# Optimization experiments

Measured on AMD Instinct MI355X. Metric: run time of the kernel, lower is better.

Reference implementation:

```python
import jax, jax.numpy as jnp
import numpy as np

TOPK = 0.1  # fraction of h*w spatial positions, from __init__ default


def setup_inputs() -> dict:
    key = jax.random.key(0)
    x = jax.random.normal(key, (32, 256, 56, 56), dtype=jnp.float32)
    return {"x": x}


def reference(x) -> jnp.ndarray:
    # Faithful translation of TopKLayer.sparse_hw (including its quirky
    # comparison of ascending *ranks* against the spatial *index* of the
    # k-th largest element, exactly as the torch code does).
    n, c, h, w = x.shape
    k = int(max(1, TOPK * h * w))  # topk_keep_num = 313 for 56x56
    x_r = x.reshape(n * c, h * w)              # (nc, hw)
    abs_x = jnp.abs(x_r)
    # ranks[i, j] = ascending rank of abs_x[i, j] within row i
    ranks = jnp.argsort(jnp.argsort(abs_x, axis=1), axis=1)
    # spatial index of the k-th largest |x| in each row
    thr_idx = jax.lax.top_k(abs_x, k)[1][:, -1]  # (nc,)
    mask = (ranks < thr_idx[:, None]).reshape(n, c, h, w)
    return x * mask.astype(x.dtype)
```

## Files before the change

### kernel.cpp

```cpp
#include <hip/hip_runtime.h>
#include <stdint.h>


#define HW     3136
#define NT     128
#define WPB    2
#define KSEL   313u
#define CAP    448
#define CAP2   64
#define SLICE  1088
#define O_CAND 0
#define O_HC   448
#define O_TINY 704
#define M31    0x7fffffffu

__device__ __forceinline__ unsigned wscan_incl(unsigned v) {
    const int lane = threadIdx.x & 63;
#pragma unroll
    for (int d = 1; d < 64; d <<= 1) {
        unsigned o = __shfl_up(v, d, 64);
        if (lane >= d) v += o;
    }
    return v;
}

__device__ __forceinline__ unsigned bcast_first(unsigned flag, unsigned val) {
    unsigned long long bal = __ballot(flag != 0);
    int fl = __ffsll(bal) - 1;
    return __shfl(val, fl, 64);
}

__device__ __forceinline__ void hadd(unsigned* h, unsigned b) {
    atomicAdd(&h[(b >> 1) + (b >> 5)], (b & 1) ? 0x10000u : 1u);
}

template <bool fromTop>
__device__ __forceinline__ void wave_select(
        unsigned* sl, const unsigned* __restrict__ gx,
        const uint4* v, unsigned vx,
        const unsigned* pc, unsigned base,
        unsigned rank, unsigned& keyOut, unsigned& idxOut) {
    const int lane = threadIdx.x & 63;

    unsigned packed1 = 0;
    {
        unsigned run = base;
#pragma unroll
        for (int i = 0; i < 32; ++i) {
            const unsigned cb = (i & 1) ? (pc[i >> 1] >> 16) : (pc[i >> 1] & 0xFFFFu);
            if (fromTop) {
                const unsigned suf = HW - run - cb;
                if (suf < rank && rank <= suf + cb)
                    packed1 = ((unsigned)(lane * 32 + i) << 16) | (rank - suf);
            } else {
                if (run < rank && rank <= run + cb)
                    packed1 = ((unsigned)(lane * 32 + i) << 16) | (rank - run);
            }
            run += cb;
        }
    }
    packed1 = bcast_first(packed1, packed1);
    const unsigned b0 = packed1 >> 16;
    const unsigned m1 = packed1 & 0xFFFFu;

    unsigned cc = 0;
#pragma unroll
    for (int i = 0; i < 12; ++i) {
        cc += (((v[i].x & M31) >> 20) == b0);
        cc += (((v[i].y & M31) >> 20) == b0);
        cc += (((v[i].z & M31) >> 20) == b0);
        cc += (((v[i].w & M31) >> 20) == b0);
    }
    cc += (((vx & M31) >> 20) == b0);
    const unsigned cin = wscan_incl(cc);
    const unsigned cnt = __shfl(cin, 63, 64);
    bool fb = (cnt > CAP);
    unsigned result = 0;

    if (!fb) {
        unsigned pos = cin - cc;
#pragma unroll
        for (int i = 0; i < 12; ++i) {
            const unsigned i0 = 4u * (unsigned)(lane + 64 * i);
            unsigned k;
            k = v[i].x & M31; if ((k >> 20) == b0) sl[O_CAND + pos++] = ((k & 0xFFFFFu) << 12) | i0;
            k = v[i].y & M31; if ((k >> 20) == b0) sl[O_CAND + pos++] = ((k & 0xFFFFFu) << 12) | (i0 + 1u);
            k = v[i].z & M31; if ((k >> 20) == b0) sl[O_CAND + pos++] = ((k & 0xFFFFFu) << 12) | (i0 + 2u);
            k = v[i].w & M31; if ((k >> 20) == b0) sl[O_CAND + pos++] = ((k & 0xFFFFFu) << 12) | (i0 + 3u);
        }
        { const unsigned k = vx & M31;
          if ((k >> 20) == b0) sl[O_CAND + pos++] = ((k & 0xFFFFFu) << 12) | (3072u + (unsigned)lane); }

#pragma unroll
        for (int i = 0; i < 4; ++i) sl[O_HC + lane + 64 * i] = 0;
        for (unsigned i = lane; i < cnt; i += 64)
            atomicAdd(&sl[O_HC + (sl[O_CAND + i] >> 24)], 1u);

        unsigned hh[4];
#pragma unroll
        for (int i = 0; i < 4; ++i) hh[i] = sl[O_HC + 4 * lane + i];
        const unsigned s4 = hh[0] + hh[1] + hh[2] + hh[3];
        unsigned run2 = wscan_incl(s4) - s4;
        unsigned packed2 = 0;
#pragma unroll
        for (int i = 0; i < 4; ++i) {
            if (fromTop) {
                const unsigned suf = cnt - run2 - hh[i];
                if (suf < m1 && m1 <= suf + hh[i])
                    packed2 = ((unsigned)(4 * lane + i) << 16) | (m1 - suf);
            } else {
                if (run2 < m1 && m1 <= run2 + hh[i])
                    packed2 = ((unsigned)(4 * lane + i) << 16) | (m1 - run2);
            }
            run2 += hh[i];
        }
        packed2 = bcast_first(packed2, packed2);
        const unsigned b2 = packed2 >> 16;
        const unsigned m2 = packed2 & 0xFFFFu;

        unsigned tc = 0;
        for (unsigned i = lane; i < cnt; i += 64) tc += ((sl[O_CAND + i] >> 24) == b2);
        const unsigned tincl = wscan_incl(tc);
        const unsigned c2 = __shfl(tincl, 63, 64);
        if (c2 > CAP2) fb = true;
        else {
            unsigned tpos = tincl - tc;
            for (unsigned i = lane; i < cnt; i += 64) {
                const unsigned cw = sl[O_CAND + i];
                if ((cw >> 24) == b2) sl[O_TINY + tpos++] = cw;
            }
            unsigned hitf = 0, resv = 0;
            if ((unsigned)lane < c2) {
                const unsigned ci = sl[O_TINY + lane];
                const unsigned di = fromTop ? (ci ^ 0xFFFu) : ci;
                unsigned r = 1;
                for (unsigned j = 0; j < c2; ++j) {
                    const unsigned dj = fromTop ? (sl[O_TINY + j] ^ 0xFFFu) : sl[O_TINY + j];
                    if (fromTop ? (dj > di) : (dj < di)) r++;
                }
                if (r == m2) { hitf = 1; resv = ci; }
            }
            result = bcast_first(hitf, resv);
        }
    }

    if (fb) {
        unsigned hitf = 0, resv = 0;
        for (unsigned j = lane; j < HW; j += 64) {
            const unsigned k = gx[j] & M31;
            if ((k >> 20) != b0) continue;
            unsigned Ci = ((k & 0xFFFFFu) << 12) | j;
            if (fromTop) Ci ^= 0xFFFu;
            unsigned r = 1;
            for (unsigned j2 = 0; j2 < HW; ++j2) {
                const unsigned k2 = gx[j2] & M31;
                if ((k2 >> 20) != b0) continue;
                unsigned Cj = ((k2 & 0xFFFFFu) << 12) | j2;
                if (fromTop) Cj ^= 0xFFFu;
                if (fromTop ? (Cj > Ci) : (Cj < Ci)) r++;
            }
            if (r == m1) { hitf = 1; resv = ((k & 0xFFFFFu) << 12) | j; }
        }
        result = bcast_first(hitf, resv);
    }

    keyOut = (b0 << 20) | (result >> 12);
    idxOut = result & 0xFFFu;
}

extern "C" __global__ void __launch_bounds__(NT)
topk_kernel(const float* __restrict__ x, float* __restrict__ out) {
    __shared__ unsigned lds[WPB][SLICE];
    const int lane = threadIdx.x & 63;
    const int w = threadIdx.x >> 6;
    const int row = blockIdx.x * WPB + w;
    unsigned* sl = lds[w];
    const uint4* __restrict__ xin4 = (const uint4*)(x + (size_t)row * HW);
    const unsigned* __restrict__ gx = (const unsigned*)xin4;
    uint4* __restrict__ xout4 = (uint4*)(out + (size_t)row * HW);
    unsigned* __restrict__ gout = (unsigned*)(out + (size_t)row * HW);

#pragma unroll
    for (int i = 0; i < 17; ++i) sl[lane + 64 * i] = 0;

    uint4 v[12];
#pragma unroll
    for (int i = 0; i < 12; ++i) v[i] = xin4[lane + 64 * i];
    const unsigned vx = gx[3072 + lane];

#pragma unroll
    for (int i = 0; i < 12; ++i) {
        hadd(sl, (v[i].x & M31) >> 20);
        hadd(sl, (v[i].y & M31) >> 20);
        hadd(sl, (v[i].z & M31) >> 20);
        hadd(sl, (v[i].w & M31) >> 20);
    }
    hadd(sl, (vx & M31) >> 20);

    unsigned pc[16];
#pragma unroll
    for (int i = 0; i < 16; ++i) pc[i] = sl[lane * 17 + i];
    unsigned ssum = 0;
#pragma unroll
    for (int i = 0; i < 16; ++i) ssum += (pc[i] & 0xFFFFu) + (pc[i] >> 16);
    const unsigned base = wscan_incl(ssum) - ssum;

    unsigned KA, tIdx;
    wave_select<true>(sl, gx, v, vx, pc, base, KSEL, KA, tIdx);

    if (tIdx == 0) {
        const uint4 z = make_uint4(0u, 0u, 0u, 0u);
#pragma unroll
        for (int i = 0; i < 12; ++i) xout4[lane + 64 * i] = z;
        gout[3072 + lane] = 0u;
        return;
    }

    unsigned KB, eB;
    wave_select<false>(sl, gx, v, vx, pc, base, tIdx, KB, eB);

#pragma unroll
    for (int i = 0; i < 12; ++i) {
        const unsigned i0 = 4u * (unsigned)(lane + 64 * i);
        uint4 o = v[i];
        unsigned k;
        k = o.x & M31; if (!(k < KB || (k == KB && i0      <= eB))) o.x = 0u;
        k = o.y & M31; if (!(k < KB || (k == KB && i0 + 1u <= eB))) o.y = 0u;
        k = o.z & M31; if (!(k < KB || (k == KB && i0 + 2u <= eB))) o.z = 0u;
        k = o.w & M31; if (!(k < KB || (k == KB && i0 + 3u <= eB))) o.w = 0u;
        xout4[lane + 64 * i] = o;
    }
    {
        const unsigned k = vx & M31;
        gout[3072 + lane] =
            (k < KB || (k == KB && (3072u + (unsigned)lane) <= eB)) ? vx : 0u;
    }
}

extern "C" void kernel_launch(void* const* d_in, const int* in_sizes, int n_in,
                              void* d_out, int out_size, void* d_ws, size_t ws_size,
                              hipStream_t stream) {
    const float* x = (const float*)d_in[0];
    float* out = (float*)d_out;
    const int rows = in_sizes[0] / HW;
    topk_kernel<<<dim3(rows / WPB), dim3(NT), 0, stream>>>(x, out);
}
```

Before: 63.48 us.

## Process two rows per 256-thread block with block-wide radix histograms

Replaces the one-wavefront-per-row design with a 256-thread block that handles two rows jointly. Each row gets a 2048-bin histogram on the top 11 key bits, built with block-wide LDS atomics, and the two rows' bin counts are packed into 16-bit halves so a single prefix scan covers both. Candidate compaction now uses atomic counters, the refinement step runs on one wave per row, and the fallback is spread across the whole block. The goal is to cut per-thread register load and serial per-wave work, at the cost of extra __syncthreads barriers and atomic contention.

```diff
diff --git a/kernel.cpp b/kernel.cpp
--- a/kernel.cpp
+++ b/kernel.cpp
@@ -2,17 +2,17 @@
 #include <stdint.h>
 
 
-#define HW     3136
-#define NT     128
-#define WPB    2
-#define KSEL   313u
-#define CAP    448
-#define CAP2   64
-#define SLICE  1088
+#define HW    3136
+#define NW4   784
+#define NT    256
+#define KSEL  313u
+#define CAP   320u
+#define CAP2  64u
 #define O_CAND 0
-#define O_HC   448
+#define O_HC   384
 #define O_TINY 704
-#define M31    0x7fffffffu
+#define M31   0x7fffffffu
+#define SENT  0xFFFFFFFFu
 
 __device__ __forceinline__ unsigned wscan_incl(unsigned v) {
     const int lane = threadIdx.x & 63;
@@ -26,215 +26,243 @@
 
 __device__ __forceinline__ unsigned bcast_first(unsigned flag, unsigned val) {
     unsigned long long bal = __ballot(flag != 0);
-    int fl = __ffsll(bal) - 1;
-    return __shfl(val, fl, 64);
-}
-
-__device__ __forceinline__ void hadd(unsigned* h, unsigned b) {
-    atomicAdd(&h[(b >> 1) + (b >> 5)], (b & 1) ? 0x10000u : 1u);
+    if (!bal) return 0u;
+    return __shfl(val, __ffsll(bal) - 1, 64);
 }
 
 template <bool fromTop>
-__device__ __forceinline__ void wave_select(
-        unsigned* sl, const unsigned* __restrict__ gx,
-        const uint4* v, unsigned vx,
-        const unsigned* pc, unsigned base,
-        unsigned rank, unsigned& keyOut, unsigned& idxOut) {
+__device__ void wave_finish(unsigned* hr, unsigned* br) {
     const int lane = threadIdx.x & 63;
-
-    unsigned packed1 = 0;
-    {
-        unsigned run = base;
-#pragma unroll
-        for (int i = 0; i < 32; ++i) {
-            const unsigned cb = (i & 1) ? (pc[i >> 1] >> 16) : (pc[i >> 1] & 0xFFFFu);
-            if (fromTop) {
-                const unsigned suf = HW - run - cb;
-                if (suf < rank && rank <= suf + cb)
-                    packed1 = ((unsigned)(lane * 32 + i) << 16) | (rank - suf);
-            } else {
-                if (run < rank && rank <= run + cb)
-                    packed1 = ((unsigned)(lane * 32 + i) << 16) | (rank - run);
-            }
-            run += cb;
-        }
-    }
-    packed1 = bcast_first(packed1, packed1);
-    const unsigned b0 = packed1 >> 16;
-    const unsigned m1 = packed1 & 0xFFFFu;
-
-    unsigned cc = 0;
-#pragma unroll
-    for (int i = 0; i < 12; ++i) {
-        cc += (((v[i].x & M31) >> 20) == b0);
-        cc += (((v[i].y & M31) >> 20) == b0);
-        cc += (((v[i].z & M31) >> 20) == b0);
-        cc += (((v[i].w & M31) >> 20) == b0);
-    }
-    cc += (((vx & M31) >> 20) == b0);
-    const unsigned cin = wscan_incl(cc);
-    const unsigned cnt = __shfl(cin, 63, 64);
-    bool fb = (cnt > CAP);
-    unsigned result = 0;
-
-    if (!fb) {
-        unsigned pos = cin - cc;
-#pragma unroll
-        for (int i = 0; i < 12; ++i) {
-            const unsigned i0 = 4u * (unsigned)(lane + 64 * i);
-            unsigned k;
-            k = v[i].x & M31; if ((k >> 20) == b0) sl[O_CAND + pos++] = ((k & 0xFFFFFu) << 12) | i0;
-            k = v[i].y & M31; if ((k >> 20) == b0) sl[O_CAND + pos++] = ((k & 0xFFFFFu) << 12) | (i0 + 1u);
-            k = v[i].z & M31; if ((k >> 20) == b0) sl[O_CAND + pos++] = ((k & 0xFFFFFu) << 12) | (i0 + 2u);
-            k = v[i].w & M31; if ((k >> 20) == b0) sl[O_CAND + pos++] = ((k & 0xFFFFFu) << 12) | (i0 + 3u);
-        }
-        { const unsigned k = vx & M31;
-          if ((k >> 20) == b0) sl[O_CAND + pos++] = ((k & 0xFFFFFu) << 12) | (3072u + (unsigned)lane); }
-
-#pragma unroll
-        for (int i = 0; i < 4; ++i) sl[O_HC + lane + 64 * i] = 0;
-        for (unsigned i = lane; i < cnt; i += 64)
-            atomicAdd(&sl[O_HC + (sl[O_CAND + i] >> 24)], 1u);
-
-        unsigned hh[4];
-#pragma unroll
-        for (int i = 0; i < 4; ++i) hh[i] = sl[O_HC + 4 * lane + i];
-        const unsigned s4 = hh[0] + hh[1] + hh[2] + hh[3];
-        unsigned run2 = wscan_incl(s4) - s4;
-        unsigned packed2 = 0;
-#pragma unroll
-        for (int i = 0; i < 4; ++i) {
-            if (fromTop) {
-                const unsigned suf = cnt - run2 - hh[i];
-                if (suf < m1 && m1 <= suf + hh[i])
-                    packed2 = ((unsigned)(4 * lane + i) << 16) | (m1 - suf);
-            } else {
-                if (run2 < m1 && m1 <= run2 + hh[i])
-                    packed2 = ((unsigned)(4 * lane + i) << 16) | (m1 - run2);
-            }
-            run2 += hh[i];
-        }
-        packed2 = bcast_first(packed2, packed2);
-        const unsigned b2 = packed2 >> 16;
-        const unsigned m2 = packed2 & 0xFFFFu;
-
-        unsigned tc = 0;
-        for (unsigned i = lane; i < cnt; i += 64) tc += ((sl[O_CAND + i] >> 24) == b2);
-        const unsigned tincl = wscan_incl(tc);
-        const unsigned c2 = __shfl(tincl, 63, 64);
-        if (c2 > CAP2) fb = true;
-        else {
-            unsigned tpos = tincl - tc;
-            for (unsigned i = lane; i < cnt; i += 64) {
-                const unsigned cw = sl[O_CAND + i];
-                if ((cw >> 24) == b2) sl[O_TINY + tpos++] = cw;
-            }
-            unsigned hitf = 0, resv = 0;
-            if ((unsigned)lane < c2) {
-                const unsigned ci = sl[O_TINY + lane];
-                const unsigned di = fromTop ? (ci ^ 0xFFFu) : ci;
-                unsigned r = 1;
-                for (unsigned j = 0; j < c2; ++j) {
-                    const unsigned dj = fromTop ? (sl[O_TINY + j] ^ 0xFFFu) : sl[O_TINY + j];
-                    if (fromTop ? (dj > di) : (dj < di)) r++;
-                }
-                if (r == m2) { hitf = 1; resv = ci; }
-            }
-            result = bcast_first(hitf, resv);
-        }
-    }
-
-    if (fb) {
-        unsigned hitf = 0, resv = 0;
-        for (unsigned j = lane; j < HW; j += 64) {
-            const unsigned k = gx[j] & M31;
-            if ((k >> 20) != b0) continue;
-            unsigned Ci = ((k & 0xFFFFFu) << 12) | j;
-            if (fromTop) Ci ^= 0xFFFu;
-            unsigned r = 1;
-            for (unsigned j2 = 0; j2 < HW; ++j2) {
-                const unsigned k2 = gx[j2] & M31;
-                if ((k2 >> 20) != b0) continue;
-                unsigned Cj = ((k2 & 0xFFFFFu) << 12) | j2;
-                if (fromTop) Cj ^= 0xFFFu;
-                if (fromTop ? (Cj > Ci) : (Cj < Ci)) r++;
-            }
-            if (r == m1) { hitf = 1; resv = ((k & 0xFFFFFu) << 12) | j; }
-        }
-        result = bcast_first(hitf, resv);
-    }
-
-    keyOut = (b0 << 20) | (result >> 12);
-    idxOut = result & 0xFFFu;
+    const unsigned cnt = br[3];
+    const unsigned m1  = br[1];
+    unsigned* cand = hr + O_CAND;
+    unsigned* hc   = hr + O_HC;
+    unsigned* tiny = hr + O_TINY;
+    if (cnt > CAP) { if (lane == 0) br[2] = (m1 == 0) ? 0u : SENT; return; }
+    for (unsigned i = lane; i < cnt; i += 64) atomicAdd(&hc[cand[i] >> 24], 1u);
+    unsigned hh[4];
+#pragma unroll
+    for (int i = 0; i < 4; ++i) hh[i] = hc[4 * lane + i];
+    const unsigned s4 = hh[0] + hh[1] + hh[2] + hh[3];
+    unsigned run2 = wscan_incl(s4) - s4;
+    unsigned packed2 = 0;
+#pragma unroll
+    for (int i = 0; i < 4; ++i) {
+        if (fromTop) {
+            const unsigned suf = cnt - run2 - hh[i];
+            if (suf < m1 && m1 <= suf + hh[i])
+                packed2 = ((unsigned)(4 * lane + i) << 16) | (m1 - suf);
+        } else {
+            if (run2 < m1 && m1 <= run2 + hh[i])
+                packed2 = ((unsigned)(4 * lane + i) << 16) | (m1 - run2);
+        }
+        run2 += hh[i];
+    }
+    packed2 = bcast_first(packed2, packed2);
+    if (packed2 == 0) { if (lane == 0) br[2] = 0u; return; }
+    const unsigned b2 = packed2 >> 16;
+    const unsigned m2 = packed2 & 0xFFFFu;
+    unsigned tc = 0;
+    for (unsigned i = lane; i < cnt; i += 64) tc += ((cand[i] >> 24) == b2);
+    const unsigned tincl = wscan_incl(tc);
+    const unsigned c2 = __shfl((int)tincl, 63, 64);
+    if (c2 > CAP2) { if (lane == 0) br[2] = SENT; return; }
+    unsigned tpos = tincl - tc;
+    for (unsigned i = lane; i < cnt; i += 64) {
+        const unsigned cw = cand[i];
+        if ((cw >> 24) == b2) tiny[tpos++] = cw;
+    }
+    unsigned hitf = 0, resv = 0;
+    if ((unsigned)lane < c2) {
+        const unsigned ci = tiny[lane];
+        const unsigned di = fromTop ? (ci ^ 0xFFFu) : ci;
+        unsigned r = 1;
+        for (unsigned j = 0; j < c2; ++j) {
+            const unsigned dj = fromTop ? (tiny[j] ^ 0xFFFu) : tiny[j];
+            if (fromTop ? (dj > di) : (dj < di)) r++;
+        }
+        if (r == m2) { hitf = 1; resv = ci; }
+    }
+    resv = bcast_first(hitf, resv);
+    if (lane == 0) br[2] = resv;
+}
+
+template <bool fromTop>
+__device__ void block_fallback(const unsigned* __restrict__ gx, unsigned* br) {
+    const unsigned b0 = br[0], m1 = br[1];
+    const int t = threadIdx.x;
+    for (int j = t; j < HW; j += NT) {
+        const unsigned k = gx[j] & M31;
+        if ((k >> 20) != b0) continue;
+        unsigned Ci = ((k & 0xFFFFFu) << 12) | (unsigned)j;
+        if (fromTop) Ci ^= 0xFFFu;
+        unsigned r = 1;
+        for (int j2 = 0; j2 < HW; ++j2) {
+            const unsigned k2 = gx[j2] & M31;
+            if ((k2 >> 20) != b0) continue;
+            unsigned Cj = ((k2 & 0xFFFFFu) << 12) | (unsigned)j2;
+            if (fromTop) Cj ^= 0xFFFu;
+            if (fromTop ? (Cj > Ci) : (Cj < Ci)) r++;
+        }
+        if (r == m1) br[2] = ((k & 0xFFFFFu) << 12) | (unsigned)j;
+    }
 }
 
 extern "C" __global__ void __launch_bounds__(NT)
 topk_kernel(const float* __restrict__ x, float* __restrict__ out) {
-    __shared__ unsigned lds[WPB][SLICE];
-    const int lane = threadIdx.x & 63;
-    const int w = threadIdx.x >> 6;
-    const int row = blockIdx.x * WPB + w;
-    unsigned* sl = lds[w];
-    const uint4* __restrict__ xin4 = (const uint4*)(x + (size_t)row * HW);
-    const unsigned* __restrict__ gx = (const unsigned*)xin4;
-    uint4* __restrict__ xout4 = (uint4*)(out + (size_t)row * HW);
-    unsigned* __restrict__ gout = (unsigned*)(out + (size_t)row * HW);
-
-#pragma unroll
-    for (int i = 0; i < 17; ++i) sl[lane + 64 * i] = 0;
-
-    uint4 v[12];
-#pragma unroll
-    for (int i = 0; i < 12; ++i) v[i] = xin4[lane + 64 * i];
-    const unsigned vx = gx[3072 + lane];
-
-#pragma unroll
-    for (int i = 0; i < 12; ++i) {
-        hadd(sl, (v[i].x & M31) >> 20);
-        hadd(sl, (v[i].y & M31) >> 20);
-        hadd(sl, (v[i].z & M31) >> 20);
-        hadd(sl, (v[i].w & M31) >> 20);
-    }
-    hadd(sl, (vx & M31) >> 20);
-
-    unsigned pc[16];
-#pragma unroll
-    for (int i = 0; i < 16; ++i) pc[i] = sl[lane * 17 + i];
+    __shared__ unsigned s_h0[2048];
+    __shared__ unsigned s_h1[2048];
+    __shared__ unsigned s_warp[4];
+    __shared__ unsigned s_b0[4];
+    __shared__ unsigned s_b1[4];
+
+    const int t = threadIdx.x;
+    const int lane = t & 63;
+    const int wid = t >> 6;
+    const size_t r0 = (size_t)blockIdx.x * 2;
+    const uint4* __restrict__ xin0 = (const uint4*)(x + r0 * HW);
+    const uint4* __restrict__ xin1 = (const uint4*)(x + (r0 + 1) * HW);
+    uint4* __restrict__ xo0 = (uint4*)(out + r0 * HW);
+    uint4* __restrict__ xo1 = (uint4*)(out + (r0 + 1) * HW);
+    const unsigned* __restrict__ gx0 = (const unsigned*)xin0;
+    const unsigned* __restrict__ gx1 = (const unsigned*)xin1;
+
+    {
+        const uint4 z = make_uint4(0u, 0u, 0u, 0u);
+        ((uint4*)s_h0)[t] = z; ((uint4*)s_h0)[t + NT] = z;
+        ((uint4*)s_h1)[t] = z; ((uint4*)s_h1)[t + NT] = z;
+    }
+    __syncthreads();
+
+    const bool has3 = (t < NW4 - 3 * NT);
+    uint4 va[4], vb[4];
+#pragma unroll
+    for (int i = 0; i < 3; ++i) { va[i] = xin0[t + i * NT]; vb[i] = xin1[t + i * NT]; }
+    va[3] = has3 ? xin0[t + 3 * NT] : make_uint4(0u, 0u, 0u, 0u);
+    vb[3] = has3 ? xin1[t + 3 * NT] : make_uint4(0u, 0u, 0u, 0u);
+#pragma unroll
+    for (int i = 0; i < 4; ++i) {
+        if (i == 3 && !has3) break;
+        atomicAdd(&s_h0[(va[i].x & M31) >> 20], 1u);
+        atomicAdd(&s_h0[(va[i].y & M31) >> 20], 1u);
+        atomicAdd(&s_h0[(va[i].z & M31) >> 20], 1u);
+        atomicAdd(&s_h0[(va[i].w & M31) >> 20], 1u);
+        atomicAdd(&s_h1[(vb[i].x & M31) >> 20], 1u);
+        atomicAdd(&s_h1[(vb[i].y & M31) >> 20], 1u);
+        atomicAdd(&s_h1[(vb[i].z & M31) >> 20], 1u);
+        atomicAdd(&s_h1[(vb[i].w & M31) >> 20], 1u);
+    }
+    __syncthreads();
+
+    const uint4 ha = ((const uint4*)s_h0)[2 * t], hb = ((const uint4*)s_h0)[2 * t + 1];
+    const uint4 hc = ((const uint4*)s_h1)[2 * t], hd = ((const uint4*)s_h1)[2 * t + 1];
+    unsigned c01[8] = { ha.x | (hc.x << 16), ha.y | (hc.y << 16),
+                        ha.z | (hc.z << 16), ha.w | (hc.w << 16),
+                        hb.x | (hd.x << 16), hb.y | (hd.y << 16),
+                        hb.z | (hd.z << 16), hb.w | (hd.w << 16) };
     unsigned ssum = 0;
 #pragma unroll
-    for (int i = 0; i < 16; ++i) ssum += (pc[i] & 0xFFFFu) + (pc[i] >> 16);
-    const unsigned base = wscan_incl(ssum) - ssum;
-
-    unsigned KA, tIdx;
-    wave_select<true>(sl, gx, v, vx, pc, base, KSEL, KA, tIdx);
-
-    if (tIdx == 0) {
-        const uint4 z = make_uint4(0u, 0u, 0u, 0u);
-#pragma unroll
-        for (int i = 0; i < 12; ++i) xout4[lane + 64 * i] = z;
-        gout[3072 + lane] = 0u;
-        return;
-    }
-
-    unsigned KB, eB;
-    wave_select<false>(sl, gx, v, vx, pc, base, tIdx, KB, eB);
-
-#pragma unroll
-    for (int i = 0; i < 12; ++i) {
-        const unsigned i0 = 4u * (unsigned)(lane + 64 * i);
-        uint4 o = v[i];
-        unsigned k;
-        k = o.x & M31; if (!(k < KB || (k == KB && i0      <= eB))) o.x = 0u;
-        k = o.y & M31; if (!(k < KB || (k == KB && i0 + 1u <= eB))) o.y = 0u;
-        k = o.z & M31; if (!(k < KB || (k == KB && i0 + 2u <= eB))) o.z = 0u;
-        k = o.w & M31; if (!(k < KB || (k == KB && i0 + 3u <= eB))) o.w = 0u;
-        xout4[lane + 64 * i] = o;
-    }
+    for (int i = 0; i < 8; ++i) ssum += c01[i];
+    const unsigned Si = wscan_incl(ssum);
+    if (lane == 63) s_warp[wid] = Si;
+    __syncthreads();
+
+    unsigned cross = 0;
+    for (int w2 = 0; w2 < wid; ++w2) cross += s_warp[w2];
+    const unsigned base01 = cross + Si - ssum;
     {
-        const unsigned k = vx & M31;
-        gout[3072 + lane] =
-            (k < KB || (k == KB && (3072u + (unsigned)lane) <= eB)) ? vx : 0u;
-    }
+        unsigned run0 = base01 & 0xFFFFu, run1 = base01 >> 16;
+#pragma unroll
+        for (int i = 0; i < 8; ++i) {
+            const unsigned c0 = c01[i] & 0xFFFFu, c1 = c01[i] >> 16;
+            const unsigned suf0 = HW - run0 - c0;
+            if (suf0 < KSEL && KSEL <= suf0 + c0) { s_b0[0] = 8u*(unsigned)t + (unsigned)i; s_b0[1] = KSEL - suf0; }
+            const unsigned suf1 = HW - run1 - c1;
+            if (suf1 < KSEL && KSEL <= suf1 + c1) { s_b1[0] = 8u*(unsigned)t + (unsigned)i; s_b1[1] = KSEL - suf1; }
+            run0 += c0; run1 += c1;
+        }
+    }
+    if (t == 0) { s_b0[3] = 0; s_b1[3] = 0; }
+    s_h0[O_HC + t] = 0; s_h1[O_HC + t] = 0;
+    __syncthreads();
+
+    auto compact = [&](const uint4* v, unsigned b0, unsigned* br, unsigned* cand) {
+#pragma unroll
+        for (int i = 0; i < 4; ++i) {
+            if (i == 3 && !has3) break;
+            const unsigned i0 = 4u * (unsigned)(t + i * NT);
+            unsigned k, p;
+            k = v[i].x & M31; if ((k >> 20) == b0) { p = atomicAdd(&br[3], 1u); if (p < CAP) cand[p] = ((k & 0xFFFFFu) << 12) | i0; }
+            k = v[i].y & M31; if ((k >> 20) == b0) { p = atomicAdd(&br[3], 1u); if (p < CAP) cand[p] = ((k & 0xFFFFFu) << 12) | (i0 + 1u); }
+            k = v[i].z & M31; if ((k >> 20) == b0) { p = atomicAdd(&br[3], 1u); if (p < CAP) cand[p] = ((k & 0xFFFFFu) << 12) | (i0 + 2u); }
+            k = v[i].w & M31; if ((k >> 20) == b0) { p = atomicAdd(&br[3], 1u); if (p < CAP) cand[p] = ((k & 0xFFFFFu) << 12) | (i0 + 3u); }
+        }
+    };
+    compact(va, s_b0[0], s_b0, s_h0 + O_CAND);
+    compact(vb, s_b1[0], s_b1, s_h1 + O_CAND);
+    __syncthreads();
+
+    if (wid == 0) wave_finish<true>(s_h0, s_b0);
+    else if (wid == 1) wave_finish<true>(s_h1, s_b1);
+    __syncthreads();
+
+    unsigned compA0 = s_b0[2], compA1 = s_b1[2];
+    if (compA0 == SENT) { block_fallback<true>(gx0, s_b0); __syncthreads(); compA0 = s_b0[2]; }
+    if (compA1 == SENT) { block_fallback<true>(gx1, s_b1); __syncthreads(); compA1 = s_b1[2]; }
+    const unsigned tIdx0 = compA0 & 0xFFFu;
+    const unsigned tIdx1 = compA1 & 0xFFFu;
+
+    {
+        unsigned run0 = base01 & 0xFFFFu, run1 = base01 >> 16;
+#pragma unroll
+        for (int i = 0; i < 8; ++i) {
+            const unsigned c0 = c01[i] & 0xFFFFu, c1 = c01[i] >> 16;
+            if (run0 < tIdx0 && tIdx0 <= run0 + c0) { s_b0[0] = 8u*(unsigned)t + (unsigned)i; s_b0[1] = tIdx0 - run0; }
+            if (run1 < tIdx1 && tIdx1 <= run1 + c1) { s_b1[0] = 8u*(unsigned)t + (unsigned)i; s_b1[1] = tIdx1 - run1; }
+            run0 += c0; run1 += c1;
+        }
+    }
+    if (t == 0) {
+        s_b0[3] = 0; s_b1[3] = 0;
+        if (tIdx0 == 0) { s_b0[0] = 0; s_b0[1] = 0; }
+        if (tIdx1 == 0) { s_b1[0] = 0; s_b1[1] = 0; }
+    }
+    s_h0[O_HC + t] = 0; s_h1[O_HC + t] = 0;
+    __syncthreads();
+
+    const unsigned b0B0 = s_b0[0], b0B1 = s_b1[0];
+    compact(va, b0B0, s_b0, s_h0 + O_CAND);
+    compact(vb, b0B1, s_b1, s_h1 + O_CAND);
+    __syncthreads();
+
+    if (wid == 0) wave_finish<false>(s_h0, s_b0);
+    else if (wid == 1) wave_finish<false>(s_h1, s_b1);
+    __syncthreads();
+
+    unsigned compB0 = s_b0[2], compB1 = s_b1[2];
+    if (compB0 == SENT) { block_fallback<false>(gx0, s_b0); __syncthreads(); compB0 = s_b0[2]; }
+    if (compB1 == SENT) { block_fallback<false>(gx1, s_b1); __syncthreads(); compB1 = s_b1[2]; }
+    const unsigned KB0 = (b0B0 << 20) | (compB0 >> 12);
+    const unsigned eB0 = compB0 & 0xFFFu;
+    const unsigned KB1 = (b0B1 << 20) | (compB1 >> 12);
+    const unsigned eB1 = compB1 & 0xFFFu;
+
+    auto store_row = [&](const uint4* v, uint4* xo, unsigned KB, unsigned eB) {
+#pragma unroll
+        for (int i = 0; i < 4; ++i) {
+            if (i == 3 && !has3) break;
+            const unsigned i0 = 4u * (unsigned)(t + i * NT);
+            uint4 o = v[i];
+            unsigned k;
+            k = o.x & M31; if (!(k < KB || (k == KB && i0      <= eB))) o.x = 0u;
+            k = o.y & M31; if (!(k < KB || (k == KB && i0 + 1u <= eB))) o.y = 0u;
+            k = o.z & M31; if (!(k < KB || (k == KB && i0 + 2u <= eB))) o.z = 0u;
+            k = o.w & M31; if (!(k < KB || (k == KB && i0 + 3u <= eB))) o.w = 0u;
+            xo[t + i * NT] = o;
+        }
+    };
+    store_row(va, xo0, KB0, eB0);
+    store_row(vb, xo1, KB1, eB1);
 }
 
 extern "C" void kernel_launch(void* const* d_in, const int* in_sizes, int n_in,
@@ -243,5 +271,5 @@
     const float* x = (const float*)d_in[0];
     float* out = (float*)d_out;
     const int rows = in_sizes[0] / HW;
-    topk_kernel<<<dim3(rows / WPB), dim3(NT), 0, stream>>>(x, out);
-}
+    topk_kernel<<<dim3(rows / 2), dim3(NT), 0, stream>>>(x, out);
+}
```

Measured after the change: 69.42 us. 9.4% more time.
